# Kernel optimization log

Hardware: AMD Instinct MI355X
Metric: run time of the kernel (lower is better)

## Reference

```python
import jax, jax.numpy as jnp
import numpy as np

# YOLOv4 stride-8 head config (yolov4.cfg)
ALL_ANCHORS = [[12,16],[19,36],[40,28],[36,75],[76,55],[72,146],[142,110],[192,243],[459,401]]
ANCHOR_MASK = [0, 1, 2]
N_CLASSES = 80
SCALE_XY = 1.2  # scale_x_y for this head
N_BBOX_ATTRS = 5  # tx, ty, tw, th, obj


def setup_inputs() -> dict:
    key = jax.random.key(0)
    attrs = N_CLASSES + N_BBOX_ATTRS  # 85
    n_anchors = len(ANCHOR_MASK)      # 3
    # raw conv output: [batch, n_anchors*attrs, grid, grid]
    x = jax.random.normal(key, (16, n_anchors * attrs, 76, 76), dtype=jnp.float32)
    return {"x": x, "input_dim": 608}


def reference(x, input_dim):
    B = x.shape[0]
    G = x.shape[2]                      # grid_dim (INPUT_H_DIM)
    stride = input_dim // G             # grid_stride
    A = len(ANCHOR_MASK)
    attrs = N_CLASSES + N_BBOX_ATTRS

    # anchors scaled to grid units: [A, 2]
    anc = jnp.asarray([ALL_ANCHORS[i] for i in ANCHOR_MASK], dtype=jnp.float32) / stride

    # [B, A, attrs, H, W] -> [B, H, W, A, attrs]
    x = x.reshape(B, A, attrs, G, G).transpose(0, 3, 4, 1, 2)

    # yolo_transform: sigmoid+scale tx/ty, exp*anchor tw/th, sigmoid obj+cls
    txy = jax.nn.sigmoid(x[..., 0:2]) * SCALE_XY - (SCALE_XY - 1.0) / 2.0
    twh = jnp.exp(x[..., 2:4]) * anc            # broadcast over [B,H,W,A,2]
    objcls = jax.nn.sigmoid(x[..., 4:])

    # add_grid_offsets: torch.meshgrid(grid, grid) is 'ij' -> y_offset[i,j]=i, x_offset[i,j]=j
    gy, gx = jnp.meshgrid(jnp.arange(G), jnp.arange(G), indexing="ij")
    off = jnp.stack([gx, gy], axis=-1).astype(jnp.float32)[:, :, None, :]  # [H,W,1,2]
    txy = txy + off

    # scale bbox attrs (tx..th) to input-image pixels
    boxes = jnp.concatenate([txy, twh], axis=-1) * jnp.float32(stride)

    out = jnp.concatenate([boxes, objcls], axis=-1)  # [B,H,W,A,attrs]
    return out.reshape(B, G * G * A, attrs)
```

## Files before the change

kernel.cpp:

```cpp
#include <hip/hip_runtime.h>

#define GRIDD 76
#define NROWS 255
#define HALF  128
#define PITCH 80
#define GG    (GRIDD * GRIDD)

__global__ __launch_bounds__(512, 8) void yolo_head_kernel(
    const float* __restrict__ x, const int* __restrict__ dimp,
    float* __restrict__ out)
{
    __shared__ float lds[HALF * PITCH];
    const unsigned lb   = (blockIdx.x & 7u) * 304u + (blockIdx.x >> 3);
    const unsigned b    = lb / (GRIDD * 2);
    const unsigned hr   = lb - b * (GRIDD * 2);
    const unsigned h    = hr >> 1;
    const unsigned half = hr & 1;
    const unsigned t    = threadIdx.x;
    const unsigned rbase = half * 127u;
    const float stride = (float)(*dimp / GRIDD);

    const float* __restrict__ src = x + (size_t)b * (NROWS * GG)
                                      + (size_t)rbase * GG + (size_t)h * GRIDD;
    for (unsigned i = t; i < HALF * 19u; i += 512u) {
        unsigned row = i / 19u;
        unsigned c4  = (i - row * 19u) * 4u;
        const float4 v = *reinterpret_cast<const float4*>(
            src + (size_t)row * GG + c4);
        *reinterpret_cast<float4*>(&lds[row * PITCH + c4]) = v;
    }
    __syncthreads();

    const unsigned wid  = t >> 6;
    const unsigned lane = t & 63u;
    const float fh = (float)h;
    const float mB = -0.1f * stride;
    float* __restrict__ outbh = out + (size_t)(b * GRIDD + h) * (GRIDD * NROWS);

    for (unsigned tt = wid; tt < 38u; tt += 8u) {
        const unsigned rc = tt & 1u;
        const unsigned wc = tt >> 1;
        const unsigned r  = (rc << 6) + lane;
        const unsigned rem = rbase + r;
        const unsigned a    = (rem >= 170u) ? 2u : ((rem >= 85u) ? 1u : 0u);
        const unsigned attr = rem - a * 85u;
        const bool  wh  = (attr == 2u) | (attr == 3u);
        const bool  isx = (attr == 0u);
        float anc = 0.f;
        if (attr == 2u) anc = (a == 0u) ? 12.f : ((a == 1u) ? 19.f : 40.f);
        if (attr == 3u) anc = (a == 0u) ? 16.f : ((a == 1u) ? 36.f : 28.f);
        const float sgn = wh ? 1.f : -1.f;
        const float A   = (attr < 2u) ? 1.2f * stride : 1.f;
        const float B0  = (attr == 1u) ? (fh * stride + mB) : 0.f;

        const float4 vv = *reinterpret_cast<const float4*>(&lds[r * PITCH + wc * 4u]);
        float* __restrict__ dst = outbh + rem;
        #pragma unroll
        for (unsigned i = 0; i < 4u; ++i) {
            const float v = (i == 0) ? vv.x : (i == 1) ? vv.y : (i == 2) ? vv.z : vv.w;
            const float w = (float)(4u * wc + i);
            const float e = __expf(sgn * v);
            const float sig = __builtin_amdgcn_rcpf(1.0f + e);
            const float Bi  = isx ? fmaf(w, stride, mB) : B0;
            const float o   = wh ? e * anc : fmaf(sig, A, Bi);
            dst[(size_t)(4u * wc + i) * NROWS] = o;
        }
    }
}

extern "C" void kernel_launch(void* const* d_in, const int* in_sizes, int n_in,
                              void* d_out, int out_size, void* d_ws, size_t ws_size,
                              hipStream_t stream) {
    const float* x  = (const float*)d_in[0];
    const int* dimp = (const int*)d_in[1];
    float* out      = (float*)d_out;
    const int B = in_sizes[0] / (NROWS * GG);
    yolo_head_kernel<<<B * GRIDD * 2, 512, 0, stream>>>(x, dimp, out);
}
```

Measured before the change: 37.85 us.

## Make kernel persistent with double-buffered async global-to-LDS staging

Replaces one-block-per-(batch,row,half) launch with 512 persistent blocks that each walk a contiguous range of work units. The next unit is staged into a second LDS buffer with global_load_lds while the current one is transformed and stored, so load latency overlaps compute. This aims to cut launch/tail overhead and exposed load latency. In exchange it lowers occupancy (launch bounds 4, double LDS), hardcodes the batch size via NUNITS/NBLK, and relies on a packed LDS layout written directly by the async loads.

```diff
diff --git a/kernel.cpp b/kernel.cpp
--- a/kernel.cpp
+++ b/kernel.cpp
@@ -1,70 +1,109 @@
 #include <hip/hip_runtime.h>
 
-#define GRIDD 76
-#define NROWS 255
-#define HALF  128
-#define PITCH 80
-#define GG    (GRIDD * GRIDD)
+#define GRIDD  76
+#define NROWS  255
+#define GG     (GRIDD * GRIDD)
+#define UROWS  128
+#define UPITCH 76
+#define UDW    (UROWS * UPITCH)
+#define NUNITS 2432
+#define NBLK   512
 
-__global__ __launch_bounds__(512, 8) void yolo_head_kernel(
+typedef __attribute__((address_space(3))) unsigned lds_u32;
+typedef __attribute__((address_space(1))) unsigned glb_u32;
+
+__device__ __forceinline__ void gll16(const float* g, float* l) {
+    __builtin_amdgcn_global_load_lds((const glb_u32*)g, (lds_u32*)l, 16, 0, 0);
+}
+
+__device__ __forceinline__ void stage_unit(const float* __restrict__ x,
+                                           unsigned u, float* buf,
+                                           unsigned wid, unsigned lane)
+{
+    const unsigned b    = u / 152u;
+    const unsigned hr   = u - b * 152u;
+    const unsigned h    = hr >> 1;
+    const unsigned half = hr & 1u;
+    const float* src = x + (size_t)b * (NROWS * GG)
+                         + (size_t)(half * 127u) * GG + (size_t)h * GRIDD;
+    #pragma unroll
+    for (unsigned k = 0; k < 5u; ++k) {
+        unsigned i = k * 512u + (wid << 6) + lane;
+        if (i < 2432u) {
+            unsigned row = i / 19u;
+            unsigned c4  = (i - row * 19u) << 2;
+            gll16(src + (size_t)row * GG + c4,
+                  buf + (size_t)((wid << 6) + k * 512u) * 4u);
+        }
+    }
+}
+
+__global__ __launch_bounds__(512, 4) void yolo_head_kernel(
     const float* __restrict__ x, const int* __restrict__ dimp,
     float* __restrict__ out)
 {
-    __shared__ float lds[HALF * PITCH];
-    const unsigned lb   = (blockIdx.x & 7u) * 304u + (blockIdx.x >> 3);
-    const unsigned b    = lb / (GRIDD * 2);
-    const unsigned hr   = lb - b * (GRIDD * 2);
-    const unsigned h    = hr >> 1;
-    const unsigned half = hr & 1;
+    __shared__ float buf[2][UDW];
+    const unsigned lb   = (blockIdx.x & 7u) * 64u + (blockIdx.x >> 3);
     const unsigned t    = threadIdx.x;
-    const unsigned rbase = half * 127u;
-    const float stride = (float)(*dimp / GRIDD);
+    const unsigned wid  = t >> 6;
+    const unsigned lane = t & 63u;
+    const float stride  = (float)(*dimp / GRIDD);
+    const float mB      = -0.1f * stride;
 
-    const float* __restrict__ src = x + (size_t)b * (NROWS * GG)
-                                      + (size_t)rbase * GG + (size_t)h * GRIDD;
-    for (unsigned i = t; i < HALF * 19u; i += 512u) {
-        unsigned row = i / 19u;
-        unsigned c4  = (i - row * 19u) * 4u;
-        const float4 v = *reinterpret_cast<const float4*>(
-            src + (size_t)row * GG + c4);
-        *reinterpret_cast<float4*>(&lds[row * PITCH + c4]) = v;
-    }
+    const unsigned u0 = (lb * 19u) >> 2;
+    const unsigned u1 = ((lb + 1u) * 19u) >> 2;
+
+    stage_unit(x, u0, buf[0], wid, lane);
     __syncthreads();
 
-    const unsigned wid  = t >> 6;
-    const unsigned lane = t & 63u;
-    const float fh = (float)h;
-    const float mB = -0.1f * stride;
-    float* __restrict__ outbh = out + (size_t)(b * GRIDD + h) * (GRIDD * NROWS);
+    unsigned p = 0;
+    for (unsigned u = u0; u < u1; ++u) {
+        if (u + 1u < u1)
+            stage_unit(x, u + 1u, buf[p ^ 1u], wid, lane);
 
-    for (unsigned tt = wid; tt < 38u; tt += 8u) {
-        const unsigned rc = tt & 1u;
-        const unsigned wc = tt >> 1;
-        const unsigned r  = (rc << 6) + lane;
-        const unsigned rem = rbase + r;
-        const unsigned a    = (rem >= 170u) ? 2u : ((rem >= 85u) ? 1u : 0u);
-        const unsigned attr = rem - a * 85u;
-        const bool  wh  = (attr == 2u) | (attr == 3u);
-        const bool  isx = (attr == 0u);
-        float anc = 0.f;
-        if (attr == 2u) anc = (a == 0u) ? 12.f : ((a == 1u) ? 19.f : 40.f);
-        if (attr == 3u) anc = (a == 0u) ? 16.f : ((a == 1u) ? 36.f : 28.f);
-        const float sgn = wh ? 1.f : -1.f;
-        const float A   = (attr < 2u) ? 1.2f * stride : 1.f;
-        const float B0  = (attr == 1u) ? (fh * stride + mB) : 0.f;
+        const unsigned b    = u / 152u;
+        const unsigned hr   = u - b * 152u;
+        const unsigned h    = hr >> 1;
+        const unsigned rbase = (hr & 1u) * 127u;
+        const float fh = (float)h;
+        float* __restrict__ outbh = out + (size_t)(b * GRIDD + h) * (GRIDD * NROWS);
+        const float* bc = buf[p];
 
-        const float4 vv = *reinterpret_cast<const float4*>(&lds[r * PITCH + wc * 4u]);
-        float* __restrict__ dst = outbh + rem;
         #pragma unroll
-        for (unsigned i = 0; i < 4u; ++i) {
-            const float v = (i == 0) ? vv.x : (i == 1) ? vv.y : (i == 2) ? vv.z : vv.w;
-            const float w = (float)(4u * wc + i);
-            const float e = __expf(sgn * v);
-            const float sig = __builtin_amdgcn_rcpf(1.0f + e);
-            const float Bi  = isx ? fmaf(w, stride, mB) : B0;
-            const float o   = wh ? e * anc : fmaf(sig, A, Bi);
-            dst[(size_t)(4u * wc + i) * NROWS] = o;
+        for (unsigned j = 0; j < 5u; ++j) {
+            unsigned tt = wid + (j << 3);
+            if (tt < 38u) {
+                const unsigned rc  = tt & 1u;
+                const unsigned wc  = tt >> 1;
+                const unsigned r   = (rc << 6) + lane;
+                const unsigned rem = rbase + r;
+                const unsigned a    = (rem >= 170u) ? 2u : ((rem >= 85u) ? 1u : 0u);
+                const unsigned attr = rem - a * 85u;
+                const bool  wh  = (attr == 2u) | (attr == 3u);
+                const bool  isx = (attr == 0u);
+                float anc = 0.f;
+                if (attr == 2u) anc = (a == 0u) ? 12.f : ((a == 1u) ? 19.f : 40.f);
+                if (attr == 3u) anc = (a == 0u) ? 16.f : ((a == 1u) ? 36.f : 28.f);
+                const float sgn = wh ? 1.f : -1.f;
+                const float A   = (attr < 2u) ? 1.2f * stride : 1.f;
+                const float B0  = (attr == 1u) ? (fh * stride + mB) : 0.f;
+
+                const float4 vv = *reinterpret_cast<const float4*>(&bc[r * UPITCH + (wc << 2)]);
+                float* __restrict__ dst = outbh + rem;
+                #pragma unroll
+                for (unsigned i = 0; i < 4u; ++i) {
+                    const float v = (i == 0) ? vv.x : (i == 1) ? vv.y : (i == 2) ? vv.z : vv.w;
+                    const float w = (float)((wc << 2) + i);
+                    const float e = __expf(sgn * v);
+                    const float sig = __builtin_amdgcn_rcpf(1.0f + e);
+                    const float Bi  = isx ? fmaf(w, stride, mB) : B0;
+                    const float o   = wh ? e * anc : fmaf(sig, A, Bi);
+                    dst[(size_t)((wc << 2) + i) * NROWS] = o;
+                }
+            }
         }
+        __syncthreads();
+        p ^= 1u;
     }
 }
 
@@ -74,6 +113,5 @@
     const float* x  = (const float*)d_in[0];
     const int* dimp = (const int*)d_in[1];
     float* out      = (float*)d_out;
-    const int B = in_sizes[0] / (NROWS * GG);
-    yolo_head_kernel<<<B * GRIDD * 2, 512, 0, stream>>>(x, dimp, out);
+    yolo_head_kernel<<<NBLK, 512, 0, stream>>>(x, dimp, out);
 }
```

Result: slower. 41.27 us (+9.0%).
